# Kernel optimization log

Hardware: AMD Instinct MI355X
Metric: run time of the kernel (lower is better)

Reference implementation:

```python
import jax, jax.numpy as jnp
import numpy as np
from jax import lax

EPS = 1e-6
C = 192
SHAPE = (2, C, 32, 48, 48)


def setup_inputs() -> dict:
    key = jax.random.key(0)
    ks = jax.random.split(key, 20)
    d = {
        "xs": jax.random.normal(ks[0], SHAPE, jnp.float32),
        "xt": jax.random.normal(ks[1], SHAPE, jnp.float32),
        "ln_w": jnp.ones((C,), jnp.float32),
        "ln_b": jnp.zeros((C,), jnp.float32),
        "qk_sp_w": jax.random.normal(ks[2], (C,), jnp.float32) * 0.1,
        "qk_sp_b": jax.random.normal(ks[3], (C,), jnp.float32) * 0.1,
        "v_sp_w": jax.random.normal(ks[4], (C,), jnp.float32) * 0.1,
        "v_sp_b": jax.random.normal(ks[5], (C,), jnp.float32) * 0.1,
        "qk_tm_w": jax.random.normal(ks[6], (C,), jnp.float32) * 0.1,
        "qk_tm_b": jax.random.normal(ks[7], (C,), jnp.float32) * 0.1,
        "v_tm_w": jax.random.normal(ks[8], (C,), jnp.float32) * 0.1,
        "v_tm_b": jax.random.normal(ks[9], (C,), jnp.float32) * 0.1,
        "attn_w": jax.random.normal(ks[10], (C, 1, 4, 4, 4), jnp.float32) * 0.1,
        "attn_b": jax.random.normal(ks[11], (C,), jnp.float32) * 0.1,
        "grn_gamma": jax.random.normal(ks[12], (1, C, 1, 1, 1), jnp.float32) * 0.1,
        "grn_beta": jax.random.normal(ks[13], (1, C, 1, 1, 1), jnp.float32) * 0.1,
        "proj_w": jax.random.normal(ks[14], (C,), jnp.float32) * 0.1,
        "proj_b": jax.random.normal(ks[15], (C,), jnp.float32) * 0.1,
    }
    return d


def _cvec(v):  # [C] -> broadcastable over [B,C,D,H,W]
    return v[None, :, None, None, None]


def _dw1(x, w, b):  # depthwise 1x1x1 conv == per-channel affine
    return x * _cvec(w) + _cvec(b)


def _ln_cf(x, w, b):  # channels-first LayerNorm over channel dim
    mean = jnp.mean(x, axis=1, keepdims=True)
    var = jnp.mean((x - mean) ** 2, axis=1, keepdims=True)
    y = (x - mean) * lax.rsqrt(var + EPS)
    return _cvec(w) * y + _cvec(b)


def _grn(x, gamma, beta):
    gx = jnp.sqrt(jnp.sum(x * x, axis=(2, 3, 4), keepdims=True))  # [B,C,1,1,1]
    nx = gx / (jnp.mean(gx, axis=1, keepdims=True) + EPS)
    return gamma * (x * nx) + beta + x


def reference(xs, xt, ln_w, ln_b, qk_sp_w, qk_sp_b, v_sp_w, v_sp_b,
              qk_tm_w, qk_tm_b, v_tm_w, v_tm_b, attn_w, attn_b,
              grn_gamma, grn_beta, proj_w, proj_b):
    x0 = xs
    xsn = _ln_cf(xs, ln_w, ln_b)
    qk = _dw1(xsn, qk_sp_w, qk_sp_b) + _dw1(xt, qk_tm_w, qk_tm_b)
    v = _dw1(xsn, v_sp_w, v_sp_b) + _dw1(xt, v_tm_w, v_tm_b)
    a = jax.nn.silu(qk)
    # depthwise 4x4x4 conv, padding 3, dilation 2 (spatial-size preserving)
    a = lax.conv_general_dilated(
        a, attn_w, window_strides=(1, 1, 1), padding=[(3, 3)] * 3,
        rhs_dilation=(2, 2, 2),
        dimension_numbers=("NCDHW", "OIDHW", "NCDHW"),
        feature_group_count=a.shape[1]) + _cvec(attn_b)
    x = a * v
    x = _grn(x, grn_gamma, grn_beta)
    x = _dw1(x, proj_w, proj_b)  # proj conv; DropPath(0) is identity
    return x0 + x
```

## Files before the change

kernel.cpp:

```cpp
#include <hip/hip_runtime.h>
#include <math.h>

#define BB 2
#define CC 192
#define DD 32
#define HH 48
#define WW 48
#define HWs (HH*WW)
#define SS (DD*HH*WW)
#define BS (BB*SS)
#define NTOT (BB*CC*SS)
#define EPSV 1e-6f

typedef unsigned short ushort;

__device__ __forceinline__ ushort pack_bf16(float x) {
    unsigned u = __float_as_uint(x);
    u += 0x7FFFu + ((u >> 16) & 1u);
    return (ushort)(u >> 16);
}
__device__ __forceinline__ unsigned pack_bf16x2(float lo, float hi) {
    return (unsigned)pack_bf16(lo) | ((unsigned)pack_bf16(hi) << 16);
}
__device__ __forceinline__ float bf16_lo(unsigned u) { return __uint_as_float(u << 16); }
__device__ __forceinline__ float bf16_hi(unsigned u) { return __uint_as_float(u & 0xFFFF0000u); }

__global__ __launch_bounds__(256) void k1_ln_av(
    const float* __restrict__ xs, const float* __restrict__ xt,
    const float* __restrict__ ln_w, const float* __restrict__ ln_b,
    const float* __restrict__ qk_sp_w, const float* __restrict__ qk_sp_b,
    const float* __restrict__ v_sp_w, const float* __restrict__ v_sp_b,
    const float* __restrict__ qk_tm_w, const float* __restrict__ qk_tm_b,
    const float* __restrict__ v_tm_w, const float* __restrict__ v_tm_b,
    ushort* __restrict__ a_out, ushort* __restrict__ v_out)
{
    __shared__ float w_all[10][CC];
    int tid = threadIdx.x;
    if (tid < CC) {
        w_all[0][tid] = ln_w[tid];    w_all[1][tid] = ln_b[tid];
        w_all[2][tid] = qk_sp_w[tid]; w_all[3][tid] = qk_sp_b[tid];
        w_all[4][tid] = qk_tm_w[tid]; w_all[5][tid] = qk_tm_b[tid];
        w_all[6][tid] = v_sp_w[tid];  w_all[7][tid] = v_sp_b[tid];
        w_all[8][tid] = v_tm_w[tid];  w_all[9][tid] = v_tm_b[tid];
    }
    __syncthreads();

    int p0 = blockIdx.x * 512;
    int b = p0 / SS;
    int s = (p0 % SS) + tid * 2;

    const float* xsp = xs + (size_t)b * CC * SS + s;
    const float* xtp = xt + (size_t)b * CC * SS + s;

    float sum0 = 0.f, sum1 = 0.f, ssum0 = 0.f, ssum1 = 0.f;
    #pragma unroll 4
    for (int c = 0; c < CC; ++c) {
        float2 v = *(const float2*)(xsp + (size_t)c * SS);
        sum0 += v.x; ssum0 += v.x * v.x;
        sum1 += v.y; ssum1 += v.y * v.y;
    }
    float mean0 = sum0 * (1.0f / CC), mean1 = sum1 * (1.0f / CC);
    float rstd0 = rsqrtf(ssum0 * (1.0f / CC) - mean0 * mean0 + EPSV);
    float rstd1 = rsqrtf(ssum1 * (1.0f / CC) - mean1 * mean1 + EPSV);

    ushort* ap = a_out + (size_t)b * CC * SS + s;
    ushort* vp = v_out + (size_t)b * CC * SS + s;
    #pragma unroll 4
    for (int c = 0; c < CC; ++c) {
        float2 v = *(const float2*)(xsp + (size_t)c * SS);
        float2 t = *(const float2*)(xtp + (size_t)c * SS);
        float xn0 = (v.x - mean0) * rstd0 * w_all[0][c] + w_all[1][c];
        float xn1 = (v.y - mean1) * rstd1 * w_all[0][c] + w_all[1][c];
        float qk0 = xn0 * w_all[2][c] + w_all[3][c] + t.x * w_all[4][c] + w_all[5][c];
        float qk1 = xn1 * w_all[2][c] + w_all[3][c] + t.y * w_all[4][c] + w_all[5][c];
        float vv0 = xn0 * w_all[6][c] + w_all[7][c] + t.x * w_all[8][c] + w_all[9][c];
        float vv1 = xn1 * w_all[6][c] + w_all[7][c] + t.y * w_all[8][c] + w_all[9][c];
        float a0 = qk0 / (1.f + __expf(-qk0));
        float a1 = qk1 / (1.f + __expf(-qk1));
        *(unsigned*)(ap + (size_t)c * SS) = pack_bf16x2(a0, a1);
        *(unsigned*)(vp + (size_t)c * SS) = pack_bf16x2(vv0, vv1);
    }
}

#define ODT 4
#define OHT 24
#define NP 10
#define NR 30
#define RSD 28
#define PSD (NR*RSD)
#define TILE_DW (NP*PSD)

__global__ __launch_bounds__(576, 2) void k2_conv(
    const ushort* __restrict__ a_in, const ushort* __restrict__ v_in,
    const float* __restrict__ attn_w, const float* __restrict__ attn_b,
    ushort* __restrict__ x_out, float* __restrict__ ssq)
{
    __shared__ unsigned tile[TILE_DW];
    __shared__ float wts[64];
    int tid = threadIdx.x;
    int blk = blockIdx.x;
    int bc = blk >> 4;
    int rem = blk & 15;
    int d0 = (rem >> 1) * ODT;
    int h0 = (rem & 1) * OHT;
    int c = bc % CC;

    const ushort* abase = a_in + (size_t)bc * SS;
    for (int i2 = tid; i2 < TILE_DW / 2; i2 += 576) {
        int i = i2 * 2;
        int p = i / PSD;
        int r2 = i - p * PSD;
        int r = r2 / RSD;
        int q2 = r2 - r * RSD;
        int id = d0 - 3 + p;
        int ih = h0 - 3 + r;
        int iw = q2 * 2 - 4;
        uint2 val = make_uint2(0u, 0u);
        if ((unsigned)id < (unsigned)DD && (unsigned)ih < (unsigned)HH &&
            (unsigned)iw < 45u)
            val = *(const uint2*)(abase + (size_t)id * HWs + ih * WW + iw);
        *(uint2*)&tile[i] = val;
    }
    if (tid < 64) wts[tid] = attn_w[c * 64 + tid];
    __syncthreads();
    float bias = attn_b[c];

    int strip = tid % 6;
    int ohl = (tid / 6) % 24;
    int odl = tid / 144;
    int ow0 = strip * 8;

    float acc[8];
    #pragma unroll
    for (int j = 0; j < 8; ++j) acc[j] = 0.f;

    #pragma unroll
    for (int kd = 0; kd < 4; ++kd) {
        int p = odl + 2 * kd;
        #pragma unroll
        for (int kh = 0; kh < 4; ++kh) {
            int r = ohl + 2 * kh;
            int bd = p * PSD + r * RSD + strip * 4;
            unsigned u[8];
            *(uint4*)&u[0] = *(const uint4*)&tile[bd];
            *(uint4*)&u[4] = *(const uint4*)&tile[bd + 4];
            float wf[16];
            #pragma unroll
            for (int m = 0; m < 8; ++m) {
                wf[2*m]   = bf16_lo(u[m]);
                wf[2*m+1] = bf16_hi(u[m]);
            }
            float4 wv = *(const float4*)&wts[(kd * 4 + kh) * 4];
            #pragma unroll
            for (int j = 0; j < 8; ++j) {
                float a0 = fmaf(wf[j + 1], wv.x, acc[j]);
                float a1 = fmaf(wf[j + 3], wv.y, a0);
                float a2 = fmaf(wf[j + 5], wv.z, a1);
                acc[j]   = fmaf(wf[j + 7], wv.w, a2);
            }
        }
    }

    int od = d0 + odl, oh = h0 + ohl;
    size_t g = (size_t)bc * SS + (size_t)od * HWs + oh * WW + ow0;
    unsigned uv[4];
    *(uint4*)&uv[0] = *(const uint4*)(v_in + g);
    float ssql = 0.f;
    ushort pk[8];
    #pragma unroll
    for (int m = 0; m < 4; ++m) {
        float v0 = bf16_lo(uv[m]);
        float v1 = bf16_hi(uv[m]);
        float x0 = (acc[2*m]     + bias) * v0;
        float x1 = (acc[2*m + 1] + bias) * v1;
        ssql += x0 * x0 + x1 * x1;
        pk[2*m]     = pack_bf16(x0);
        pk[2*m + 1] = pack_bf16(x1);
    }
    *(uint4*)&x_out[g] = *(uint4*)&pk[0];

    #pragma unroll
    for (int off = 32; off > 0; off >>= 1)
        ssql += __shfl_down(ssql, off);
    if ((tid & 63) == 0) atomicAdd(&ssq[bc], ssql);
}

__global__ __launch_bounds__(384) void k3_scale(
    const float* __restrict__ ssq,
    const float* __restrict__ grn_gamma, const float* __restrict__ grn_beta,
    const float* __restrict__ proj_w, const float* __restrict__ proj_b,
    float* __restrict__ AB)
{
    __shared__ float gxs[BB*CC];
    __shared__ float msum[BB];
    int tid = threadIdx.x;
    float gx = sqrtf(ssq[tid]);
    gxs[tid] = gx;
    __syncthreads();
    if (tid < BB) {
        float s = 0.f;
        for (int c2 = 0; c2 < CC; ++c2) s += gxs[tid * CC + c2];
        msum[tid] = s * (1.0f / CC);
    }
    __syncthreads();
    int b = tid / CC, c2 = tid % CC;
    float nx = gx / (msum[b] + EPSV);
    float A  = proj_w[c2] * (1.f + grn_gamma[c2] * nx);
    float B2 = proj_w[c2] * grn_beta[c2] + proj_b[c2];
    AB[tid] = A;
    AB[BB*CC + tid] = B2;
}

__global__ __launch_bounds__(256) void k4_final(
    const float* __restrict__ xs, const ushort* __restrict__ xv,
    const float* __restrict__ AB, float* __restrict__ out)
{
    int i = blockIdx.x * 256 + threadIdx.x;
    size_t g = (size_t)i * 8;
    int bc = (int)(g / SS);
    float A  = AB[bc];
    float B2 = AB[BB*CC + bc];
    uint4 xr = *(const uint4*)&xv[g];
    unsigned hx[4];
    *(uint4*)hx = xr;
    float4 s0 = *(const float4*)&xs[g];
    float4 s1 = *(const float4*)&xs[g + 4];
    float o[8];
    float sv[8] = {s0.x, s0.y, s0.z, s0.w, s1.x, s1.y, s1.z, s1.w};
    #pragma unroll
    for (int m = 0; m < 4; ++m) {
        o[2*m]   = fmaf(A, bf16_lo(hx[m]), sv[2*m])   + B2;
        o[2*m+1] = fmaf(A, bf16_hi(hx[m]), sv[2*m+1]) + B2;
    }
    *(float4*)&out[g]     = ((float4*)o)[0];
    *(float4*)&out[g + 4] = ((float4*)o)[1];
}

extern "C" void kernel_launch(void* const* d_in, const int* in_sizes, int n_in,
                              void* d_out, int out_size, void* d_ws, size_t ws_size,
                              hipStream_t stream) {
    const float* xs      = (const float*)d_in[0];
    const float* xt      = (const float*)d_in[1];
    const float* ln_w    = (const float*)d_in[2];
    const float* ln_b    = (const float*)d_in[3];
    const float* qk_sp_w = (const float*)d_in[4];
    const float* qk_sp_b = (const float*)d_in[5];
    const float* v_sp_w  = (const float*)d_in[6];
    const float* v_sp_b  = (const float*)d_in[7];
    const float* qk_tm_w = (const float*)d_in[8];
    const float* qk_tm_b = (const float*)d_in[9];
    const float* v_tm_w  = (const float*)d_in[10];
    const float* v_tm_b  = (const float*)d_in[11];
    const float* attn_w  = (const float*)d_in[12];
    const float* attn_b  = (const float*)d_in[13];
    const float* grn_g   = (const float*)d_in[14];
    const float* grn_b   = (const float*)d_in[15];
    const float* proj_w  = (const float*)d_in[16];
    const float* proj_b  = (const float*)d_in[17];
    float* out = (float*)d_out;

    ushort* a_buf = (ushort*)d_ws;
    ushort* v_buf = a_buf + (size_t)NTOT;
    ushort* x_buf = v_buf + (size_t)NTOT;
    float* ssq    = (float*)(x_buf + (size_t)NTOT);
    float* AB     = ssq + BB*CC;

    hipMemsetAsync(ssq, 0, BB*CC*sizeof(float), stream);

    k1_ln_av<<<BS/512, 256, 0, stream>>>(xs, xt, ln_w, ln_b,
        qk_sp_w, qk_sp_b, v_sp_w, v_sp_b,
        qk_tm_w, qk_tm_b, v_tm_w, v_tm_b, a_buf, v_buf);

    k2_conv<<<BB*CC*16, 576, 0, stream>>>(a_buf, v_buf,
        attn_w, attn_b, x_buf, ssq);

    k3_scale<<<1, 384, 0, stream>>>(ssq, grn_g, grn_b, proj_w, proj_b, AB);

    k4_final<<<NTOT/8/256, 256, 0, stream>>>(xs, x_buf, AB, out);
}
```

Measured before the change: 708.8 us.

## Split LayerNorm channel reduction across warps and shrink conv tiles

The LayerNorm/activation kernel now gives each block 128 spatial positions and has four wavefront-groups each reduce 48 channels, combining partial sums through shared memory. This quadruples the block count and shortens each thread's serial channel loop. The dilated conv kernel shrinks its output tile from 24 to 16 rows, giving 24 blocks of 384 threads per channel instead of 16 blocks of 576. The conv change improves wave balance and occupancy at the cost of more halo reloads per output.

```diff
diff --git a/kernel.cpp b/kernel.cpp
--- a/kernel.cpp
+++ b/kernel.cpp
@@ -25,6 +25,7 @@
 __device__ __forceinline__ float bf16_lo(unsigned u) { return __uint_as_float(u << 16); }
 __device__ __forceinline__ float bf16_hi(unsigned u) { return __uint_as_float(u & 0xFFFF0000u); }
 
+#define CG 48
 __global__ __launch_bounds__(256) void k1_ln_av(
     const float* __restrict__ xs, const float* __restrict__ xt,
     const float* __restrict__ ln_w, const float* __restrict__ ln_b,
@@ -35,6 +36,7 @@
     ushort* __restrict__ a_out, ushort* __restrict__ v_out)
 {
     __shared__ float w_all[10][CC];
+    __shared__ float2 sred[2][4][64];
     int tid = threadIdx.x;
     if (tid < CC) {
         w_all[0][tid] = ln_w[tid];    w_all[1][tid] = ln_b[tid];
@@ -45,30 +47,41 @@
     }
     __syncthreads();
 
-    int p0 = blockIdx.x * 512;
+    int tx = tid & 63, wy = tid >> 6;
+    int p0 = blockIdx.x * 128;
     int b = p0 / SS;
-    int s = (p0 % SS) + tid * 2;
-
-    const float* xsp = xs + (size_t)b * CC * SS + s;
-    const float* xtp = xt + (size_t)b * CC * SS + s;
-
-    float sum0 = 0.f, sum1 = 0.f, ssum0 = 0.f, ssum1 = 0.f;
+    int s = (p0 % SS) + tx * 2;
+
+    const float* xsp = xs + ((size_t)b * CC + wy * CG) * SS + s;
+    const float* xtp = xt + ((size_t)b * CC + wy * CG) * SS + s;
+
+    float2 sum = make_float2(0.f, 0.f), ssum = make_float2(0.f, 0.f);
+    #pragma unroll 8
+    for (int i = 0; i < CG; ++i) {
+        float2 v = *(const float2*)(xsp + (size_t)i * SS);
+        sum.x += v.x; ssum.x += v.x * v.x;
+        sum.y += v.y; ssum.y += v.y * v.y;
+    }
+    sred[0][wy][tx] = sum;
+    sred[1][wy][tx] = ssum;
+    __syncthreads();
+    float2 S = make_float2(0.f, 0.f), Q = make_float2(0.f, 0.f);
+    #pragma unroll
+    for (int w = 0; w < 4; ++w) {
+        float2 a = sred[0][w][tx]; S.x += a.x; S.y += a.y;
+        float2 q = sred[1][w][tx]; Q.x += q.x; Q.y += q.y;
+    }
+    float mean0 = S.x * (1.0f / CC), mean1 = S.y * (1.0f / CC);
+    float rstd0 = rsqrtf(Q.x * (1.0f / CC) - mean0 * mean0 + EPSV);
+    float rstd1 = rsqrtf(Q.y * (1.0f / CC) - mean1 * mean1 + EPSV);
+
+    ushort* ap = a_out + ((size_t)b * CC + wy * CG) * SS + s;
+    ushort* vp = v_out + ((size_t)b * CC + wy * CG) * SS + s;
     #pragma unroll 4
-    for (int c = 0; c < CC; ++c) {
-        float2 v = *(const float2*)(xsp + (size_t)c * SS);
-        sum0 += v.x; ssum0 += v.x * v.x;
-        sum1 += v.y; ssum1 += v.y * v.y;
-    }
-    float mean0 = sum0 * (1.0f / CC), mean1 = sum1 * (1.0f / CC);
-    float rstd0 = rsqrtf(ssum0 * (1.0f / CC) - mean0 * mean0 + EPSV);
-    float rstd1 = rsqrtf(ssum1 * (1.0f / CC) - mean1 * mean1 + EPSV);
-
-    ushort* ap = a_out + (size_t)b * CC * SS + s;
-    ushort* vp = v_out + (size_t)b * CC * SS + s;
-    #pragma unroll 4
-    for (int c = 0; c < CC; ++c) {
-        float2 v = *(const float2*)(xsp + (size_t)c * SS);
-        float2 t = *(const float2*)(xtp + (size_t)c * SS);
+    for (int i = 0; i < CG; ++i) {
+        int c = wy * CG + i;
+        float2 v = *(const float2*)(xsp + (size_t)i * SS);
+        float2 t = *(const float2*)(xtp + (size_t)i * SS);
         float xn0 = (v.x - mean0) * rstd0 * w_all[0][c] + w_all[1][c];
         float xn1 = (v.y - mean1) * rstd1 * w_all[0][c] + w_all[1][c];
         float qk0 = xn0 * w_all[2][c] + w_all[3][c] + t.x * w_all[4][c] + w_all[5][c];
@@ -77,20 +90,20 @@
         float vv1 = xn1 * w_all[6][c] + w_all[7][c] + t.y * w_all[8][c] + w_all[9][c];
         float a0 = qk0 / (1.f + __expf(-qk0));
         float a1 = qk1 / (1.f + __expf(-qk1));
-        *(unsigned*)(ap + (size_t)c * SS) = pack_bf16x2(a0, a1);
-        *(unsigned*)(vp + (size_t)c * SS) = pack_bf16x2(vv0, vv1);
+        *(unsigned*)(ap + (size_t)i * SS) = pack_bf16x2(a0, a1);
+        *(unsigned*)(vp + (size_t)i * SS) = pack_bf16x2(vv0, vv1);
     }
 }
 
 #define ODT 4
-#define OHT 24
+#define OHT 16
 #define NP 10
-#define NR 30
+#define NR 22
 #define RSD 28
 #define PSD (NR*RSD)
 #define TILE_DW (NP*PSD)
 
-__global__ __launch_bounds__(576, 2) void k2_conv(
+__global__ __launch_bounds__(384, 2) void k2_conv(
     const ushort* __restrict__ a_in, const ushort* __restrict__ v_in,
     const float* __restrict__ attn_w, const float* __restrict__ attn_b,
     ushort* __restrict__ x_out, float* __restrict__ ssq)
@@ -99,14 +112,14 @@
     __shared__ float wts[64];
     int tid = threadIdx.x;
     int blk = blockIdx.x;
-    int bc = blk >> 4;
-    int rem = blk & 15;
-    int d0 = (rem >> 1) * ODT;
-    int h0 = (rem & 1) * OHT;
+    int bc = blk / 24;
+    int rem = blk % 24;
+    int d0 = (rem / 3) * ODT;
+    int h0 = (rem % 3) * OHT;
     int c = bc % CC;
 
     const ushort* abase = a_in + (size_t)bc * SS;
-    for (int i2 = tid; i2 < TILE_DW / 2; i2 += 576) {
+    for (int i2 = tid; i2 < TILE_DW / 2; i2 += 384) {
         int i = i2 * 2;
         int p = i / PSD;
         int r2 = i - p * PSD;
@@ -126,8 +139,8 @@
     float bias = attn_b[c];
 
     int strip = tid % 6;
-    int ohl = (tid / 6) % 24;
-    int odl = tid / 144;
+    int ohl = (tid / 6) % 16;
+    int odl = tid / 96;
     int ow0 = strip * 8;
 
     float acc[8];
@@ -267,11 +280,11 @@
 
     hipMemsetAsync(ssq, 0, BB*CC*sizeof(float), stream);
 
-    k1_ln_av<<<BS/512, 256, 0, stream>>>(xs, xt, ln_w, ln_b,
+    k1_ln_av<<<BS/128, 256, 0, stream>>>(xs, xt, ln_w, ln_b,
         qk_sp_w, qk_sp_b, v_sp_w, v_sp_b,
         qk_tm_w, qk_tm_b, v_tm_w, v_tm_b, a_buf, v_buf);
 
-    k2_conv<<<BB*CC*16, 576, 0, stream>>>(a_buf, v_buf,
+    k2_conv<<<BB*CC*24, 384, 0, stream>>>(a_buf, v_buf,
         attn_w, attn_b, x_buf, ssq);
 
     k3_scale<<<1, 384, 0, stream>>>(ssq, grn_g, grn_b, proj_w, proj_b, AB);
```

Result: faster. 665.5 us (-6.1%).
